# Kernel optimization log

Hardware: AMD Instinct MI355X
Metric: run time of the kernel (lower is better)

The kernel has to match this reference:

```python
import jax, jax.numpy as jnp
import numpy as np

N = 262144   # total nodes
E = 1048576  # total edges
B = 512      # graphs per batch
IN, H, EDIM, AH, CH, NB = 8, 128, 4, 128, 128, 4

def _lin(key, fi, fo):
    # kaiming_normal fan_out/relu approximated with fan_in scaling (only affects init stats)
    return jax.random.normal(key, (fi, fo), jnp.float32) * np.sqrt(2.0 / fi)

def setup_inputs() -> dict:
    key = jax.random.key(0)
    ks = jax.random.split(key, 24)
    inp = {}
    inp['x'] = jax.random.normal(ks[0], (N, IN), jnp.float32)
    inp['edge_index'] = jax.random.randint(ks[1], (2, E), 0, N)
    inp['edge_attr'] = jax.random.normal(ks[2], (E, EDIM), jnp.float32)
    seg = N // B
    inp['batch'] = (jnp.arange(N) // seg).astype(jnp.int32)
    inp['ptr'] = (jnp.arange(B + 1) * seg).astype(jnp.int32)
    dims = [(IN, H), (H, H), (H, H)]  # final layer outputs embed_dim == H
    for l, (di, do) in enumerate(dims):
        inp[f'We{l}'] = _lin(ks[3 + 2 * l], EDIM, di)
        inp[f'be{l}'] = jnp.zeros((di,), jnp.float32)
        inp[f'W{l}'] = _lin(ks[4 + 2 * l], di, do)
        inp[f'b{l}'] = jnp.zeros((do,), jnp.float32)
    inp['laW1'] = _lin(ks[10], H, AH); inp['lab1'] = jnp.zeros((AH,), jnp.float32)
    inp['laW2'] = _lin(ks[11], AH, 1); inp['lab2'] = jnp.zeros((1,), jnp.float32)
    inp['maW1'] = _lin(ks[12], H, AH); inp['mab1'] = jnp.zeros((AH,), jnp.float32)
    inp['maW2'] = _lin(ks[13], AH, NB); inp['mab2'] = jnp.zeros((NB,), jnp.float32)
    inp['lcW1'] = _lin(ks[14], H, CH); inp['lcb1'] = jnp.zeros((CH,), jnp.float32)
    inp['lcW2'] = _lin(ks[15], CH, 1); inp['lcb2'] = jnp.zeros((1,), jnp.float32)
    inp['mcW1'] = _lin(ks[16], H, CH); inp['mcb1'] = jnp.zeros((CH,), jnp.float32)
    inp['mcW2'] = _lin(ks[17], CH, 1); inp['mcb2'] = jnp.zeros((1,), jnp.float32)
    return inp

def _gnn(x, edge_index, edge_attr, Wes, bes, Ws, bs):
    # GINE-style edge-conditioned message passing (dropout off / eval mode)
    src, dst = edge_index[0], edge_index[1]
    h = x
    for We, be, W, b in zip(Wes, bes, Ws, bs):
        msg = jax.nn.relu(h[src] + edge_attr @ We + be)            # [E, d]
        agg = jax.ops.segment_sum(msg, dst, num_segments=N)        # [N, d]
        h = jax.nn.relu((h + agg) @ W + b)
    return h

def reference(x, edge_index, edge_attr, batch, ptr,
              We0, be0, W0, b0, We1, be1, W1, b1, We2, be2, W2, b2,
              laW1, lab1, laW2, lab2, maW1, mab1, maW2, mab2,
              lcW1, lcb1, lcW2, lcb2, mcW1, mcb1, mcW2, mcb2):
    emb = _gnn(x, edge_index, edge_attr, [We0, We1, We2], [be0, be1, be2], [W0, W1, W2], [b0, b1, b2])  # [N, H]

    # per-node location logit, then fused segmented softmax over each graph's nodes
    loc_logits = (jax.nn.relu(emb @ laW1 + lab1) @ laW2 + lab2)[:, 0]  # [N]
    seg_max = jax.ops.segment_max(loc_logits, batch, num_segments=B)
    shifted = loc_logits - seg_max[batch]
    denom = jax.ops.segment_sum(jnp.exp(shifted), batch, num_segments=B)
    logp = shifted - jnp.log(denom)[batch]                              # per-node log-prob within its graph
    loc_entropy = -jax.ops.segment_sum(jnp.exp(logp) * logp, batch, num_segments=B)  # [B]

    # segmented categorical sampling via Gumbel-max (global node index, matching start+local_idx)
    key = jax.random.key(42)
    u = jax.random.uniform(key, (N,), minval=1e-6, maxval=1.0 - 1e-6)
    pert = loc_logits - jnp.log(-jnp.log(u))
    pmax = jax.ops.segment_max(pert, batch, num_segments=B)
    cand = jnp.where(pert >= pmax[batch], jnp.arange(N), N)
    locations = jax.ops.segment_min(cand, batch, num_segments=B)        # [B] global indices
    loc_log_probs = logp[locations]                                     # [B]

    sel = emb[locations]                                                # [B, H]
    mut_logits = jax.nn.relu(sel @ maW1 + mab1) @ maW2 + mab2           # [B, NB]
    mut_logp = jax.nn.log_softmax(mut_logits, axis=-1)
    mutations = jax.random.categorical(jax.random.fold_in(key, 1), mut_logits, axis=-1)  # [B]
    mut_log_probs = jnp.take_along_axis(mut_logp, mutations[:, None], axis=-1)[:, 0]
    mut_entropy = -jnp.sum(jnp.exp(mut_logp) * mut_logp, axis=-1)

    # critics: global_add_pool + MLP -> scalar per graph; mutation critic on selected node
    pooled = jax.ops.segment_sum(emb, batch, num_segments=B)            # [B, H]
    loc_values = (jax.nn.relu(pooled @ lcW1 + lcb1) @ lcW2 + lcb2)[:, 0]
    mut_values = (jax.nn.relu(sel @ mcW1 + mcb1) @ mcW2 + mcb2)[:, 0]

    return (locations, mutations, loc_log_probs, mut_log_probs,
            loc_entropy, mut_entropy, loc_values, mut_values, emb)
```

## Files before the change

kernel.cpp:

```cpp
#include <hip/hip_runtime.h>
#include <cstdint>
#include <cstddef>

#define NN 262144
#define EE 1048576
#define BB 512
#define SEG 512

__device__ __forceinline__ unsigned rotl32(unsigned x, int r) {
    return (x << r) | (x >> (32 - r));
}

__device__ __forceinline__ void tf2x32(unsigned k0, unsigned k1, unsigned x0, unsigned x1,
                                       unsigned& o0, unsigned& o1) {
    unsigned ks[3] = {k0, k1, k0 ^ k1 ^ 0x1BD11BDAu};
    x0 += ks[0]; x1 += ks[1];
    const int R0[4] = {13, 15, 26, 6};
    const int R1[4] = {17, 29, 16, 24};
#pragma unroll
    for (int i = 0; i < 5; ++i) {
        const int* R = (i & 1) ? R1 : R0;
#pragma unroll
        for (int j = 0; j < 4; ++j) {
            x0 += x1;
            x1 = rotl32(x1, R[j]);
            x1 ^= x0;
        }
        x0 += ks[(i + 1) % 3];
        x1 += ks[(i + 2) % 3] + (unsigned)(i + 1);
    }
    o0 = x0; o1 = x1;
}

__device__ __forceinline__ float unif_loc(unsigned idx) {
    unsigned j = idx & (NN / 2 - 1);
    unsigned half = idx >> 17;
    unsigned o0, o1;
    tf2x32(0u, 42u, j, j + (unsigned)(NN / 2), o0, o1);
    unsigned bits = half ? o1 : o0;
    float f = __uint_as_float((bits >> 9) | 0x3F800000u) - 1.0f;
    const float minv = 1e-6f;
    const float maxv = 1.0f - 1e-6f;
    const float span = maxv - minv;
    return fmaxf(minv, __fadd_rn(__fmul_rn(f, span), minv));
}

__global__ void csr_count(const int* __restrict__ dst, int* __restrict__ counts, int E) {
    int i = blockIdx.x * 256 + threadIdx.x;
    if (i < E) atomicAdd(&counts[dst[i]], 1);
}

__global__ void scan512(const int* __restrict__ in, int* __restrict__ outExcl, int* __restrict__ bsum) {
    __shared__ int s[512];
    int b = blockIdx.x, tid = threadIdx.x;
    int v = in[(size_t)b * 512 + tid];
    s[tid] = v;
    __syncthreads();
    for (int d = 1; d < 512; d <<= 1) {
        int add = (tid >= d) ? s[tid - d] : 0;
        __syncthreads();
        s[tid] += add;
        __syncthreads();
    }
    outExcl[(size_t)b * 512 + tid] = s[tid] - v;
    if (tid == 511) bsum[b] = s[511];
}

__global__ void scan_fix(int* __restrict__ offs, const int* __restrict__ bbase,
                         int* __restrict__ cursor, int N, int E) {
    int gid = blockIdx.x * 512 + threadIdx.x;
    int v = offs[gid] + bbase[blockIdx.x];
    offs[gid] = v;
    cursor[gid] = v;
    if (gid == 0) offs[N] = E;
}

__global__ void csr_fill(const int* __restrict__ dst, const int* __restrict__ src,
                         const float4* __restrict__ ea, int* __restrict__ cursor,
                         int* __restrict__ ssrc, float4* __restrict__ sea, int E) {
    int i = blockIdx.x * 256 + threadIdx.x;
    if (i < E) {
        int p = atomicAdd(&cursor[dst[i]], 1);
        ssrc[p] = src[i];
        sea[p] = ea[i];
    }
}

__global__ void agg_l0(const float* __restrict__ x, const int* __restrict__ ssrc,
                       const float4* __restrict__ sea, const int* __restrict__ offs,
                       const float* __restrict__ We0, const float* __restrict__ be0,
                       float* __restrict__ out) {
    __shared__ float Ws[32];
    __shared__ float bs[8];
    int tid = threadIdx.x;
    if (tid < 32) Ws[tid] = We0[tid];
    if (tid < 8) bs[tid] = be0[tid];
    __syncthreads();
    int n = blockIdx.x * 256 + tid;
    float a[8] = {0.f, 0.f, 0.f, 0.f, 0.f, 0.f, 0.f, 0.f};
    int pb = offs[n], pe = offs[n + 1];
    for (int p = pb; p < pe; ++p) {
        int s = ssrc[p];
        float4 ev = sea[p];
        float4 xa = *(const float4*)(x + (size_t)s * 8);
        float4 xb = *(const float4*)(x + (size_t)s * 8 + 4);
        float xs[8] = {xa.x, xa.y, xa.z, xa.w, xb.x, xb.y, xb.z, xb.w};
#pragma unroll
        for (int j2 = 0; j2 < 8; ++j2) {
            float m = xs[j2] + bs[j2] + ev.x * Ws[j2] + ev.y * Ws[8 + j2] +
                      ev.z * Ws[16 + j2] + ev.w * Ws[24 + j2];
            a[j2] += fmaxf(m, 0.f);
        }
    }
    float4 o0 = {a[0], a[1], a[2], a[3]};
    float4 o1 = {a[4], a[5], a[6], a[7]};
    *(float4*)(out + (size_t)n * 8) = o0;
    *(float4*)(out + (size_t)n * 8 + 4) = o1;
}

__global__ __launch_bounds__(256) void update_l0(const float* __restrict__ x,
                                                 const float* __restrict__ agg0,
                                                 const float* __restrict__ W0,
                                                 const float* __restrict__ b0,
                                                 float* __restrict__ h1) {
    __shared__ float Ws[8 * 128];
    __shared__ float bs[128];
    int tid = threadIdx.x;
#pragma unroll
    for (int i = tid; i < 1024; i += 256) Ws[i] = W0[i];
    if (tid < 128) bs[tid] = b0[tid];
    __syncthreads();
    int sub = tid >> 7;
    int c = tid & 127;
    float bias = bs[c];
    float wcol[8];
#pragma unroll
    for (int k = 0; k < 8; ++k) wcol[k] = Ws[k * 128 + c];
    int base = blockIdx.x * 128;
    for (int it = 0; it < 64; ++it) {
        int node = base + it * 2 + sub;
        const float* xp = x + (size_t)node * 8;
        const float* ap = agg0 + (size_t)node * 8;
        float4 xa = *(const float4*)xp;
        float4 xb = *(const float4*)(xp + 4);
        float4 aa = *(const float4*)ap;
        float4 ab = *(const float4*)(ap + 4);
        float t[8] = {xa.x + aa.x, xa.y + aa.y, xa.z + aa.z, xa.w + aa.w,
                      xb.x + ab.x, xb.y + ab.y, xb.z + ab.z, xb.w + ab.w};
        float acc = bias;
#pragma unroll
        for (int k = 0; k < 8; ++k) acc = fmaf(t[k], wcol[k], acc);
        h1[(size_t)node * 128 + c] = fmaxf(acc, 0.f);
    }
}

__global__ __launch_bounds__(256) void agg_l(const float2* __restrict__ h2,
                                             const int* __restrict__ ssrc,
                                             const float4* __restrict__ sea,
                                             const int* __restrict__ offs,
                                             const float* __restrict__ We,
                                             const float* __restrict__ be,
                                             float2* __restrict__ out) {
    int tid = threadIdx.x;
    int lane = tid & 63;
    int n0 = blockIdx.x * 32 + (tid >> 6) * 8;
    n0 = __builtin_amdgcn_readfirstlane(n0);
    const float2* We2 = (const float2*)We;
    float2 w0 = We2[lane], w1 = We2[64 + lane], w2 = We2[128 + lane], w3 = We2[192 + lane];
    float2 bv = ((const float2*)be)[lane];

    int b0  = __builtin_amdgcn_readfirstlane(offs[n0 + 0]);
    int nb0 = __builtin_amdgcn_readfirstlane(offs[n0 + 1]);
    int nb1 = __builtin_amdgcn_readfirstlane(offs[n0 + 2]);
    int nb2 = __builtin_amdgcn_readfirstlane(offs[n0 + 3]);
    int nb3 = __builtin_amdgcn_readfirstlane(offs[n0 + 4]);
    int nb4 = __builtin_amdgcn_readfirstlane(offs[n0 + 5]);
    int nb5 = __builtin_amdgcn_readfirstlane(offs[n0 + 6]);
    int nb6 = __builtin_amdgcn_readfirstlane(offs[n0 + 7]);
    int nb7 = __builtin_amdgcn_readfirstlane(offs[n0 + 8]);
    int pend = nb7;

    float2 acc = {0.f, 0.f};
    float2* optr = out + (size_t)n0 * 64 + lane;

#define FLUSH(pp)                                        \
    while ((pp) == nb0) {                                \
        *optr = acc;                                     \
        acc.x = 0.f; acc.y = 0.f;                        \
        optr += 64;                                      \
        nb0 = nb1; nb1 = nb2; nb2 = nb3; nb3 = nb4;      \
        nb4 = nb5; nb5 = nb6; nb6 = nb7; nb7 = 0x7FFFFFFF; \
    }

#define ACC(hv, ev)                                                                     \
    {                                                                                   \
        float mx = hv.x + bv.x + ev.x * w0.x + ev.y * w1.x + ev.z * w2.x + ev.w * w3.x; \
        float my = hv.y + bv.y + ev.x * w0.y + ev.y * w1.y + ev.z * w2.y + ev.w * w3.y; \
        acc.x += fmaxf(mx, 0.f);                                                        \
        acc.y += fmaxf(my, 0.f);                                                        \
    }

    int p = b0;
    for (; p + 8 <= pend; p += 8) {
        int s_[8];
#pragma unroll
        for (int j = 0; j < 8; ++j) s_[j] = ssrc[p + j];
        float4 e_[8];
#pragma unroll
        for (int j = 0; j < 8; ++j) e_[j] = sea[p + j];
        float2 h_[8];
#pragma unroll
        for (int j = 0; j < 8; ++j) h_[j] = h2[(size_t)s_[j] * 64 + lane];
#pragma unroll
        for (int j = 0; j < 8; ++j) {
            FLUSH(p + j)
            ACC(h_[j], e_[j])
        }
    }
    for (; p < pend; ++p) {
        FLUSH(p)
        int s0 = ssrc[p];
        float4 e0 = sea[p];
        float2 ha = h2[(size_t)s0 * 64 + lane];
        ACC(ha, e0)
    }
    FLUSH(pend)
#undef ACC
#undef FLUSH
}


typedef __attribute__((ext_vector_type(8))) short bf16x8;
typedef __attribute__((ext_vector_type(4))) float f32x4;

__device__ __forceinline__ ushort bf16r(float x) {
    unsigned u = __float_as_uint(x);
    return (ushort)((u + 0x7FFFu + ((u >> 16) & 1u)) >> 16);
}
__device__ __forceinline__ float bf2f(ushort h) {
    return __uint_as_float(((unsigned)h) << 16);
}

__global__ void pack3(const float* __restrict__ W1, const float* __restrict__ W2,
                      const float* __restrict__ LA, uint4* __restrict__ dst) {
    const float* W = (blockIdx.x == 0) ? W1 : (blockIdx.x == 1) ? W2 : LA;
    uint4* ph = dst + (size_t)blockIdx.x * 4096;
    uint4* pl = ph + 2048;
    int t = threadIdx.x;
    int l = t & 63, q = t >> 6;
    int lo = l & 15, kg = l >> 4;
    for (int i = 0; i < 8; ++i) {
        int combo = q * 8 + i;
        int kc = combo >> 3, n = combo & 7;
        ushort h8[8], l8[8];
#pragma unroll
        for (int j = 0; j < 8; ++j) {
            float wv = W[(size_t)(kc * 32 + kg * 8 + j) * 128 + n * 16 + lo];
            ushort hh = bf16r(wv);
            h8[j] = hh;
            l8[j] = bf16r(wv - bf2f(hh));
        }
        int idx = (kc * 8 + n) * 64 + l;
        ph[idx] = *(const uint4*)h8;
        pl[idx] = *(const uint4*)l8;
    }
}

__device__ __forceinline__ void load_a_frags(const float* P, const float* Q, int r0,
                                             int lo, int kg, int kc,
                                             bf16x8& ah0, bf16x8& al0,
                                             bf16x8& ah1, bf16x8& al1) {
#pragma unroll
    for (int m = 0; m < 2; ++m) {
        const float* ap = P + (size_t)(r0 + m * 16 + lo) * 128 + kc * 32 + kg * 8;
        float4 p0 = *(const float4*)ap;
        float4 p1 = *(const float4*)(ap + 4);
        if (Q) {
            const float* qp = Q + (size_t)(r0 + m * 16 + lo) * 128 + kc * 32 + kg * 8;
            float4 q0 = *(const float4*)qp;
            float4 q1 = *(const float4*)(qp + 4);
            p0.x += q0.x; p0.y += q0.y; p0.z += q0.z; p0.w += q0.w;
            p1.x += q1.x; p1.y += q1.y; p1.z += q1.z; p1.w += q1.w;
        }
        float av[8] = {p0.x, p0.y, p0.z, p0.w, p1.x, p1.y, p1.z, p1.w};
        bf16x8 ah, al;
#pragma unroll
        for (int j = 0; j < 8; ++j) {
            ushort hh = bf16r(av[j]);
            ah[j] = (short)hh;
            al[j] = (short)bf16r(av[j] - bf2f(hh));
        }
        if (m == 0) { ah0 = ah; al0 = al; } else { ah1 = ah; al1 = al; }
    }
}

__global__ __launch_bounds__(256) void gemm_mfma(const float* __restrict__ P, const float* Q,
                                                 const uint4* __restrict__ Wh,
                                                 const uint4* __restrict__ Wl,
                                                 const float* __restrict__ bias,
                                                 float* out) {
    int tid = threadIdx.x;
    int w = tid >> 6, l = tid & 63;
    int r0 = blockIdx.x * 128 + w * 32;
    int lo = l & 15, kg = l >> 4;
    const bf16x8* Bh = (const bf16x8*)Wh;
    const bf16x8* Bl = (const bf16x8*)Wl;
    f32x4 acc[2][8];
#pragma unroll
    for (int m = 0; m < 2; ++m)
#pragma unroll
        for (int n = 0; n < 8; ++n) acc[m][n] = (f32x4){0.f, 0.f, 0.f, 0.f};

    for (int kc = 0; kc < 4; ++kc) {
        bf16x8 ah0, al0, ah1, al1;
        load_a_frags(P, Q, r0, lo, kg, kc, ah0, al0, ah1, al1);
#pragma unroll
        for (int h2i = 0; h2i < 2; ++h2i) {
            bf16x8 bh[4], bl[4];
#pragma unroll
            for (int nn = 0; nn < 4; ++nn) {
                int idx = (kc * 8 + h2i * 4 + nn) * 64 + l;
                bh[nn] = Bh[idx];
                bl[nn] = Bl[idx];
            }
#pragma unroll
            for (int nn = 0; nn < 4; ++nn) {
                int n = h2i * 4 + nn;
                acc[0][n] = __builtin_amdgcn_mfma_f32_16x16x32_bf16(ah0, bh[nn], acc[0][n], 0, 0, 0);
                acc[0][n] = __builtin_amdgcn_mfma_f32_16x16x32_bf16(al0, bh[nn], acc[0][n], 0, 0, 0);
                acc[0][n] = __builtin_amdgcn_mfma_f32_16x16x32_bf16(ah0, bl[nn], acc[0][n], 0, 0, 0);
                acc[1][n] = __builtin_amdgcn_mfma_f32_16x16x32_bf16(ah1, bh[nn], acc[1][n], 0, 0, 0);
                acc[1][n] = __builtin_amdgcn_mfma_f32_16x16x32_bf16(al1, bh[nn], acc[1][n], 0, 0, 0);
                acc[1][n] = __builtin_amdgcn_mfma_f32_16x16x32_bf16(ah1, bl[nn], acc[1][n], 0, 0, 0);
            }
        }
    }
    float bv[8];
#pragma unroll
    for (int n = 0; n < 8; ++n) bv[n] = bias[n * 16 + lo];
#pragma unroll
    for (int m = 0; m < 2; ++m)
#pragma unroll
        for (int n = 0; n < 8; ++n)
#pragma unroll
            for (int v = 0; v < 4; ++v) {
                size_t g = (size_t)(r0 + m * 16 + kg * 4 + v) * 128 + n * 16 + lo;
                out[g] = fmaxf(acc[m][n][v] + bv[n], 0.f);
            }
}

__global__ __launch_bounds__(256) void gemm_logit_mfma(const float* __restrict__ P,
                                                       const uint4* __restrict__ Wh,
                                                       const uint4* __restrict__ Wl,
                                                       const float* __restrict__ bias,
                                                       const float* __restrict__ w2,
                                                       const float* __restrict__ b2,
                                                       float* __restrict__ L) {
    int tid = threadIdx.x;
    int w = tid >> 6, l = tid & 63;
    int r0 = blockIdx.x * 128 + w * 32;
    int lo = l & 15, kg = l >> 4;
    const bf16x8* Bh = (const bf16x8*)Wh;
    const bf16x8* Bl = (const bf16x8*)Wl;
    f32x4 acc[2][8];
#pragma unroll
    for (int m = 0; m < 2; ++m)
#pragma unroll
        for (int n = 0; n < 8; ++n) acc[m][n] = (f32x4){0.f, 0.f, 0.f, 0.f};

    for (int kc = 0; kc < 4; ++kc) {
        bf16x8 ah0, al0, ah1, al1;
        load_a_frags(P, (const float*)0, r0, lo, kg, kc, ah0, al0, ah1, al1);
#pragma unroll
        for (int h2i = 0; h2i < 2; ++h2i) {
            bf16x8 bh[4], bl[4];
#pragma unroll
            for (int nn = 0; nn < 4; ++nn) {
                int idx = (kc * 8 + h2i * 4 + nn) * 64 + l;
                bh[nn] = Bh[idx];
                bl[nn] = Bl[idx];
            }
#pragma unroll
            for (int nn = 0; nn < 4; ++nn) {
                int n = h2i * 4 + nn;
                acc[0][n] = __builtin_amdgcn_mfma_f32_16x16x32_bf16(ah0, bh[nn], acc[0][n], 0, 0, 0);
                acc[0][n] = __builtin_amdgcn_mfma_f32_16x16x32_bf16(al0, bh[nn], acc[0][n], 0, 0, 0);
                acc[0][n] = __builtin_amdgcn_mfma_f32_16x16x32_bf16(ah0, bl[nn], acc[0][n], 0, 0, 0);
                acc[1][n] = __builtin_amdgcn_mfma_f32_16x16x32_bf16(ah1, bh[nn], acc[1][n], 0, 0, 0);
                acc[1][n] = __builtin_amdgcn_mfma_f32_16x16x32_bf16(al1, bh[nn], acc[1][n], 0, 0, 0);
                acc[1][n] = __builtin_amdgcn_mfma_f32_16x16x32_bf16(ah1, bl[nn], acc[1][n], 0, 0, 0);
            }
        }
    }
    float bv[8], w2v[8];
#pragma unroll
    for (int n = 0; n < 8; ++n) {
        bv[n] = bias[n * 16 + lo];
        w2v[n] = w2[n * 16 + lo];
    }
    float b2v = b2[0];
#pragma unroll
    for (int m = 0; m < 2; ++m)
#pragma unroll
        for (int v = 0; v < 4; ++v) {
            float s = 0.f;
#pragma unroll
            for (int n = 0; n < 8; ++n)
                s += fmaxf(acc[m][n][v] + bv[n], 0.f) * w2v[n];
            s += __shfl_xor(s, 8);
            s += __shfl_xor(s, 4);
            s += __shfl_xor(s, 2);
            s += __shfl_xor(s, 1);
            if (lo == 0) L[r0 + m * 16 + kg * 4 + v] = s + b2v;
        }
}

__global__ void sample_k(const float* __restrict__ L, float* __restrict__ ob,
                         int* __restrict__ locInt) {
    int g = blockIdx.x, tid = threadIdx.x;
    __shared__ float sh[512];
    __shared__ float rb[256];
    __shared__ int ib[256];
    float l0 = L[g * 512 + tid];
    float l1 = L[g * 512 + 256 + tid];
    rb[tid] = fmaxf(l0, l1);
    __syncthreads();
    for (int s2 = 128; s2 > 0; s2 >>= 1) {
        if (tid < s2) rb[tid] = fmaxf(rb[tid], rb[tid + s2]);
        __syncthreads();
    }
    float mx = rb[0];
    __syncthreads();
    float s0 = l0 - mx, s1 = l1 - mx;
    sh[tid] = s0; sh[256 + tid] = s1;
    float e0 = expf(s0), e1 = expf(s1);
    rb[tid] = e0 + e1;
    __syncthreads();
    for (int s2 = 128; s2 > 0; s2 >>= 1) {
        if (tid < s2) rb[tid] += rb[tid + s2];
        __syncthreads();
    }
    float denom = rb[0];
    __syncthreads();
    rb[tid] = e0 * s0 + e1 * s1;
    __syncthreads();
    for (int s2 = 128; s2 > 0; s2 >>= 1) {
        if (tid < s2) rb[tid] += rb[tid + s2];
        __syncthreads();
    }
    float sum2 = rb[0];
    __syncthreads();
    unsigned i0 = (unsigned)(g * 512 + tid);
    unsigned i1 = i0 + 256u;
    float p0 = l0 - logf(-logf(unif_loc(i0)));
    float p1 = l1 - logf(-logf(unif_loc(i1)));
    rb[tid] = fmaxf(p0, p1);
    __syncthreads();
    for (int s2 = 128; s2 > 0; s2 >>= 1) {
        if (tid < s2) rb[tid] = fmaxf(rb[tid], rb[tid + s2]);
        __syncthreads();
    }
    float pmax = rb[0];
    __syncthreads();
    int c0 = (p0 >= pmax) ? tid : 0x7FFFFFFF;
    int c1 = (p1 >= pmax) ? (tid + 256) : 0x7FFFFFFF;
    ib[tid] = min(c0, c1);
    __syncthreads();
    for (int s2 = 128; s2 > 0; s2 >>= 1) {
        if (tid < s2) ib[tid] = min(ib[tid], ib[tid + s2]);
        __syncthreads();
    }
    if (tid == 0) {
        int li = ib[0];
        float logD = logf(denom);
        ob[g] = (float)(g * 512 + li);
        ob[1024 + g] = sh[li] - logD;
        ob[2048 + g] = logD - sum2 / denom;
        locInt[g] = g * 512 + li;
    }
}

__global__ void pool_k(const float* __restrict__ emb, float* __restrict__ pooled) {
    int g = blockIdx.x, tid = threadIdx.x;
    int c = tid & 127, rg = tid >> 7;
    __shared__ float sh[512];
    float s0 = 0.f, s1 = 0.f, s2 = 0.f, s3 = 0.f;
    const float* base = emb + ((size_t)g * 512 + (size_t)rg * 128) * 128 + c;
    for (int n = 0; n < 128; n += 4) {
        s0 += base[(size_t)(n + 0) * 128];
        s1 += base[(size_t)(n + 1) * 128];
        s2 += base[(size_t)(n + 2) * 128];
        s3 += base[(size_t)(n + 3) * 128];
    }
    sh[tid] = (s0 + s1) + (s2 + s3);
    __syncthreads();
    if (rg == 0) pooled[g * 128 + c] = sh[c] + sh[128 + c] + sh[256 + c] + sh[384 + c];
}

__global__ void heads_k(const float* __restrict__ emb, const float* __restrict__ pooled,
                        const int* __restrict__ locInt,
                        const float* __restrict__ maW1, const float* __restrict__ mab1,
                        const float* __restrict__ maW2, const float* __restrict__ mab2,
                        const float* __restrict__ lcW1, const float* __restrict__ lcb1,
                        const float* __restrict__ lcW2, const float* __restrict__ lcb2,
                        const float* __restrict__ mcW1, const float* __restrict__ mcb1,
                        const float* __restrict__ mcW2, const float* __restrict__ mcb2,
                        float* __restrict__ ob) {
    int g = blockIdx.x, tid = threadIdx.x;
    __shared__ float sel[128], pl[128];
    __shared__ float red[4][128];
    __shared__ float red1[128];
    __shared__ float mcv_sh;
    sel[tid] = emb[(size_t)locInt[g] * 128 + tid];
    pl[tid] = pooled[g * 128 + tid];
    __syncthreads();
    float h = mab1[tid];
    for (int k = 0; k < 128; ++k) h = fmaf(sel[k], maW1[k * 128 + tid], h);
    h = fmaxf(h, 0.f);
    red[0][tid] = h * maW2[tid * 4 + 0];
    red[1][tid] = h * maW2[tid * 4 + 1];
    red[2][tid] = h * maW2[tid * 4 + 2];
    red[3][tid] = h * maW2[tid * 4 + 3];
    __syncthreads();
    for (int s2 = 64; s2 > 0; s2 >>= 1) {
        if (tid < s2) {
            red[0][tid] += red[0][tid + s2];
            red[1][tid] += red[1][tid + s2];
            red[2][tid] += red[2][tid + s2];
            red[3][tid] += red[3][tid + s2];
        }
        __syncthreads();
    }
    float h2 = mcb1[tid];
    for (int k = 0; k < 128; ++k) h2 = fmaf(sel[k], mcW1[k * 128 + tid], h2);
    h2 = fmaxf(h2, 0.f);
    red1[tid] = h2 * mcW2[tid];
    __syncthreads();
    for (int s2 = 64; s2 > 0; s2 >>= 1) {
        if (tid < s2) red1[tid] += red1[tid + s2];
        __syncthreads();
    }
    if (tid == 0) mcv_sh = red1[0] + mcb2[0];
    __syncthreads();
    float h3 = lcb1[tid];
    for (int k = 0; k < 128; ++k) h3 = fmaf(pl[k], lcW1[k * 128 + tid], h3);
    h3 = fmaxf(h3, 0.f);
    red1[tid] = h3 * lcW2[tid];
    __syncthreads();
    for (int s2 = 64; s2 > 0; s2 >>= 1) {
        if (tid < s2) red1[tid] += red1[tid + s2];
        __syncthreads();
    }
    if (tid == 0) {
        float lcv = red1[0] + lcb2[0];
        float lg[4];
#pragma unroll
        for (int c = 0; c < 4; ++c) lg[c] = red[c][0] + mab2[c];
        unsigned fk0, fk1;
        tf2x32(0u, 42u, 0u, 1u, fk0, fk1);
        float gmb[4];
#pragma unroll
        for (int c = 0; c < 4; ++c) {
            unsigned m = (unsigned)(g * 4 + c);
            unsigned j = m & 1023u;
            unsigned halfb = m >> 10;
            unsigned o0, o1;
            tf2x32(fk0, fk1, j, j + 1024u, o0, o1);
            unsigned bits = halfb ? o1 : o0;
            float f = __uint_as_float((bits >> 9) | 0x3F800000u) - 1.0f;
            const float tiny = 1.17549435e-38f;
            float u = fmaxf(tiny, __fadd_rn(__fmul_rn(f, 1.0f), tiny));
            gmb[c] = -logf(-logf(u));
        }
        int best = 0;
        float bz = gmb[0] + lg[0];
#pragma unroll
        for (int c = 1; c < 4; ++c) {
            float z = gmb[c] + lg[c];
            if (z > bz) { bz = z; best = c; }
        }
        float M = fmaxf(fmaxf(lg[0], lg[1]), fmaxf(lg[2], lg[3]));
        float se = 0.f;
#pragma unroll
        for (int c = 0; c < 4; ++c) se += expf(lg[c] - M);
        float lse = M + logf(se);
        float ent = 0.f;
#pragma unroll
        for (int c = 0; c < 4; ++c) {
            float lp = lg[c] - lse;
            ent -= expf(lp) * lp;
        }
        ob[512 + g] = (float)best;
        ob[1536 + g] = lg[best] - lse;
        ob[2560 + g] = ent;
        ob[3072 + g] = lcv;
        ob[3584 + g] = mcv_sh;
    }
}

extern "C" void kernel_launch(void* const* d_in, const int* in_sizes, int n_in,
                              void* d_out, int out_size, void* d_ws, size_t ws_size,
                              hipStream_t stream) {
    const float* x   = (const float*)d_in[0];
    const int* ei    = (const int*)d_in[1];
    const float* ea  = (const float*)d_in[2];
    const float* We0 = (const float*)d_in[5];
    const float* be0 = (const float*)d_in[6];
    const float* W0  = (const float*)d_in[7];
    const float* b0  = (const float*)d_in[8];
    const float* We1 = (const float*)d_in[9];
    const float* be1 = (const float*)d_in[10];
    const float* W1  = (const float*)d_in[11];
    const float* b1  = (const float*)d_in[12];
    const float* We2 = (const float*)d_in[13];
    const float* be2 = (const float*)d_in[14];
    const float* W2  = (const float*)d_in[15];
    const float* b2  = (const float*)d_in[16];
    const float* laW1 = (const float*)d_in[17];
    const float* lab1 = (const float*)d_in[18];
    const float* laW2 = (const float*)d_in[19];
    const float* lab2 = (const float*)d_in[20];
    const float* maW1 = (const float*)d_in[21];
    const float* mab1 = (const float*)d_in[22];
    const float* maW2 = (const float*)d_in[23];
    const float* mab2 = (const float*)d_in[24];
    const float* lcW1 = (const float*)d_in[25];
    const float* lcb1 = (const float*)d_in[26];
    const float* lcW2 = (const float*)d_in[27];
    const float* lcb2 = (const float*)d_in[28];
    const float* mcW1 = (const float*)d_in[29];
    const float* mcb1 = (const float*)d_in[30];
    const float* mcW2 = (const float*)d_in[31];
    const float* mcb2 = (const float*)d_in[32];

    float* out = (float*)d_out;
    char* ws = (char*)d_ws;
    size_t off = 0;
    auto alloc = [&](size_t bytes) -> void* {
        void* p = ws + off;
        off += (bytes + 255) & ~(size_t)255;
        return p;
    };
    float* U    = (float*)alloc((size_t)NN * 128 * 4);
    int* counts = (int*)alloc((size_t)NN * 4);
    int* offs   = (int*)alloc((size_t)(NN + 1) * 4);
    int* cursor = (int*)alloc((size_t)NN * 4);
    int* ssrc   = (int*)alloc((size_t)EE * 4);
    float4* sea = (float4*)alloc((size_t)EE * 16);
    int* bsum   = (int*)alloc(512 * 4);
    int* bbase  = (int*)alloc(512 * 4);
    int* bscr   = (int*)alloc(512 * 4);
    float* Lg   = (float*)alloc((size_t)NN * 4);
    float* pooled = (float*)alloc((size_t)BB * 128 * 4);
    int* locInt = (int*)alloc((size_t)BB * 4);

    const int* src = ei;
    const int* dstA = ei + EE;
    float* V = out + 4096;
    float* agg0 = U;

    uint4* wpack = (uint4*)cursor;

    hipMemsetAsync(counts, 0, (size_t)NN * 4, stream);
    csr_count<<<EE / 256, 256, 0, stream>>>(dstA, counts, EE);
    scan512<<<NN / 512, 512, 0, stream>>>(counts, offs, bsum);
    scan512<<<1, 512, 0, stream>>>(bsum, bbase, bscr);
    scan_fix<<<NN / 512, 512, 0, stream>>>(offs, bbase, cursor, NN, EE);
    csr_fill<<<EE / 256, 256, 0, stream>>>(dstA, src, (const float4*)ea, cursor, ssrc, sea, EE);
    pack3<<<3, 256, 0, stream>>>(W1, W2, laW1, wpack);

    agg_l0<<<NN / 256, 256, 0, stream>>>(x, ssrc, sea, offs, We0, be0, agg0);
    update_l0<<<NN / 128, 256, 0, stream>>>(x, agg0, W0, b0, V);
    agg_l<<<NN / 32, 256, 0, stream>>>((const float2*)V, ssrc, sea, offs, We1, be1, (float2*)U);
    gemm_mfma<<<NN / 128, 256, 0, stream>>>(V, U, wpack, wpack + 2048, b1, U);
    agg_l<<<NN / 32, 256, 0, stream>>>((const float2*)U, ssrc, sea, offs, We2, be2, (float2*)V);
    gemm_mfma<<<NN / 128, 256, 0, stream>>>(U, V, wpack + 4096, wpack + 6144, b2, V);

    gemm_logit_mfma<<<NN / 128, 256, 0, stream>>>(V, wpack + 8192, wpack + 10240, lab1, laW2, lab2, Lg);
    sample_k<<<BB, 256, 0, stream>>>(Lg, out, locInt);

    pool_k<<<BB, 512, 0, stream>>>(V, pooled);
    heads_k<<<BB, 128, 0, stream>>>(V, pooled, locInt, maW1, mab1, maW2, mab2,
                                    lcW1, lcb1, lcW2, lcb2, mcW1, mcb1, mcW2, mcb2, out);
}
```

Baseline: 888.1 us.

## Fold self term into aggregation and enlarge MFMA GEMM row tiles

The aggregation kernel now starts each node's accumulator from its own feature row h, so it writes h+agg directly. The GEMM kernels then read a single input instead of loading and adding two matrices. Each wave of the GEMM and logit kernels now covers 64 rows instead of 32, halving the grid and reusing the loaded weight fragments across four M tiles. The larger accumulator array (128 floats) raises register pressure, and launch_bounds(256,2) constrains occupancy.

```diff
diff --git a/kernel.cpp b/kernel.cpp
--- a/kernel.cpp
+++ b/kernel.cpp
@@ -180,16 +180,26 @@
     int nb7 = __builtin_amdgcn_readfirstlane(offs[n0 + 8]);
     int pend = nb7;
 
-    float2 acc = {0.f, 0.f};
+    float2 sf1 = h2[(size_t)(n0 + 1) * 64 + lane];
+    float2 sf2 = h2[(size_t)(n0 + 2) * 64 + lane];
+    float2 sf3 = h2[(size_t)(n0 + 3) * 64 + lane];
+    float2 sf4 = h2[(size_t)(n0 + 4) * 64 + lane];
+    float2 sf5 = h2[(size_t)(n0 + 5) * 64 + lane];
+    float2 sf6 = h2[(size_t)(n0 + 6) * 64 + lane];
+    float2 sf7 = h2[(size_t)(n0 + 7) * 64 + lane];
+    float2 acc = h2[(size_t)(n0 + 0) * 64 + lane];
+
     float2* optr = out + (size_t)n0 * 64 + lane;
 
-#define FLUSH(pp)                                        \
-    while ((pp) == nb0) {                                \
-        *optr = acc;                                     \
-        acc.x = 0.f; acc.y = 0.f;                        \
-        optr += 64;                                      \
-        nb0 = nb1; nb1 = nb2; nb2 = nb3; nb3 = nb4;      \
+#define FLUSH(pp)                                          \
+    while ((pp) == nb0) {                                  \
+        *optr = acc;                                       \
+        optr += 64;                                        \
+        nb0 = nb1; nb1 = nb2; nb2 = nb3; nb3 = nb4;        \
         nb4 = nb5; nb5 = nb6; nb6 = nb7; nb7 = 0x7FFFFFFF; \
+        acc = sf1;                                         \
+        sf1 = sf2; sf2 = sf3; sf3 = sf4; sf4 = sf5;        \
+        sf5 = sf6; sf6 = sf7;                              \
     }
 
 #define ACC(hv, ev)                                                                     \
@@ -266,54 +276,46 @@
     }
 }
 
-__device__ __forceinline__ void load_a_frags(const float* P, const float* Q, int r0,
-                                             int lo, int kg, int kc,
-                                             bf16x8& ah0, bf16x8& al0,
-                                             bf16x8& ah1, bf16x8& al1) {
-#pragma unroll
-    for (int m = 0; m < 2; ++m) {
-        const float* ap = P + (size_t)(r0 + m * 16 + lo) * 128 + kc * 32 + kg * 8;
-        float4 p0 = *(const float4*)ap;
-        float4 p1 = *(const float4*)(ap + 4);
-        if (Q) {
-            const float* qp = Q + (size_t)(r0 + m * 16 + lo) * 128 + kc * 32 + kg * 8;
-            float4 q0 = *(const float4*)qp;
-            float4 q1 = *(const float4*)(qp + 4);
-            p0.x += q0.x; p0.y += q0.y; p0.z += q0.z; p0.w += q0.w;
-            p1.x += q1.x; p1.y += q1.y; p1.z += q1.z; p1.w += q1.w;
-        }
-        float av[8] = {p0.x, p0.y, p0.z, p0.w, p1.x, p1.y, p1.z, p1.w};
-        bf16x8 ah, al;
-#pragma unroll
-        for (int j = 0; j < 8; ++j) {
-            ushort hh = bf16r(av[j]);
-            ah[j] = (short)hh;
-            al[j] = (short)bf16r(av[j] - bf2f(hh));
-        }
-        if (m == 0) { ah0 = ah; al0 = al; } else { ah1 = ah; al1 = al; }
-    }
-}
-
-__global__ __launch_bounds__(256) void gemm_mfma(const float* __restrict__ P, const float* Q,
-                                                 const uint4* __restrict__ Wh,
-                                                 const uint4* __restrict__ Wl,
-                                                 const float* __restrict__ bias,
-                                                 float* out) {
+__device__ __forceinline__ void conv_frag(const float4& r0, const float4& r1,
+                                          bf16x8& ah, bf16x8& al) {
+    float av[8] = {r0.x, r0.y, r0.z, r0.w, r1.x, r1.y, r1.z, r1.w};
+#pragma unroll
+    for (int j = 0; j < 8; ++j) {
+        ushort hh = bf16r(av[j]);
+        ah[j] = (short)hh;
+        al[j] = (short)bf16r(av[j] - bf2f(hh));
+    }
+}
+
+__global__ __launch_bounds__(256, 2) void gemm_mfma(const float* P,
+                                                    const uint4* __restrict__ Wh,
+                                                    const uint4* __restrict__ Wl,
+                                                    const float* __restrict__ bias,
+                                                    float* out) {
     int tid = threadIdx.x;
     int w = tid >> 6, l = tid & 63;
-    int r0 = blockIdx.x * 128 + w * 32;
+    int r0 = blockIdx.x * 256 + w * 64;
     int lo = l & 15, kg = l >> 4;
     const bf16x8* Bh = (const bf16x8*)Wh;
     const bf16x8* Bl = (const bf16x8*)Wl;
-    f32x4 acc[2][8];
-#pragma unroll
-    for (int m = 0; m < 2; ++m)
+    f32x4 acc[4][8];
+#pragma unroll
+    for (int m = 0; m < 4; ++m)
 #pragma unroll
         for (int n = 0; n < 8; ++n) acc[m][n] = (f32x4){0.f, 0.f, 0.f, 0.f};
 
     for (int kc = 0; kc < 4; ++kc) {
-        bf16x8 ah0, al0, ah1, al1;
-        load_a_frags(P, Q, r0, lo, kg, kc, ah0, al0, ah1, al1);
+        float4 pa[8];
+#pragma unroll
+        for (int m = 0; m < 4; ++m) {
+            const float* ap = P + (size_t)(r0 + m * 16 + lo) * 128 + kc * 32 + kg * 8;
+            pa[2 * m]     = *(const float4*)ap;
+            pa[2 * m + 1] = *(const float4*)(ap + 4);
+        }
+        bf16x8 ah[4], al[4];
+#pragma unroll
+        for (int m = 0; m < 4; ++m)
+            conv_frag(pa[2 * m], pa[2 * m + 1], ah[m], al[m]);
 #pragma unroll
         for (int h2i = 0; h2i < 2; ++h2i) {
             bf16x8 bh[4], bl[4];
@@ -326,12 +328,12 @@
 #pragma unroll
             for (int nn = 0; nn < 4; ++nn) {
                 int n = h2i * 4 + nn;
-                acc[0][n] = __builtin_amdgcn_mfma_f32_16x16x32_bf16(ah0, bh[nn], acc[0][n], 0, 0, 0);
-                acc[0][n] = __builtin_amdgcn_mfma_f32_16x16x32_bf16(al0, bh[nn], acc[0][n], 0, 0, 0);
-                acc[0][n] = __builtin_amdgcn_mfma_f32_16x16x32_bf16(ah0, bl[nn], acc[0][n], 0, 0, 0);
-                acc[1][n] = __builtin_amdgcn_mfma_f32_16x16x32_bf16(ah1, bh[nn], acc[1][n], 0, 0, 0);
-                acc[1][n] = __builtin_amdgcn_mfma_f32_16x16x32_bf16(al1, bh[nn], acc[1][n], 0, 0, 0);
-                acc[1][n] = __builtin_amdgcn_mfma_f32_16x16x32_bf16(ah1, bl[nn], acc[1][n], 0, 0, 0);
+#pragma unroll
+                for (int m = 0; m < 4; ++m) {
+                    acc[m][n] = __builtin_amdgcn_mfma_f32_16x16x32_bf16(ah[m], bh[nn], acc[m][n], 0, 0, 0);
+                    acc[m][n] = __builtin_amdgcn_mfma_f32_16x16x32_bf16(al[m], bh[nn], acc[m][n], 0, 0, 0);
+                    acc[m][n] = __builtin_amdgcn_mfma_f32_16x16x32_bf16(ah[m], bl[nn], acc[m][n], 0, 0, 0);
+                }
             }
         }
     }
@@ -339,7 +341,7 @@
 #pragma unroll
     for (int n = 0; n < 8; ++n) bv[n] = bias[n * 16 + lo];
 #pragma unroll
-    for (int m = 0; m < 2; ++m)
+    for (int m = 0; m < 4; ++m)
 #pragma unroll
         for (int n = 0; n < 8; ++n)
 #pragma unroll
@@ -349,28 +351,37 @@
             }
 }
 
-__global__ __launch_bounds__(256) void gemm_logit_mfma(const float* __restrict__ P,
-                                                       const uint4* __restrict__ Wh,
-                                                       const uint4* __restrict__ Wl,
-                                                       const float* __restrict__ bias,
-                                                       const float* __restrict__ w2,
-                                                       const float* __restrict__ b2,
-                                                       float* __restrict__ L) {
+__global__ __launch_bounds__(256, 2) void gemm_logit_mfma(const float* __restrict__ P,
+                                                          const uint4* __restrict__ Wh,
+                                                          const uint4* __restrict__ Wl,
+                                                          const float* __restrict__ bias,
+                                                          const float* __restrict__ w2,
+                                                          const float* __restrict__ b2,
+                                                          float* __restrict__ L) {
     int tid = threadIdx.x;
     int w = tid >> 6, l = tid & 63;
-    int r0 = blockIdx.x * 128 + w * 32;
+    int r0 = blockIdx.x * 256 + w * 64;
     int lo = l & 15, kg = l >> 4;
     const bf16x8* Bh = (const bf16x8*)Wh;
     const bf16x8* Bl = (const bf16x8*)Wl;
-    f32x4 acc[2][8];
-#pragma unroll
-    for (int m = 0; m < 2; ++m)
+    f32x4 acc[4][8];
+#pragma unroll
+    for (int m = 0; m < 4; ++m)
 #pragma unroll
         for (int n = 0; n < 8; ++n) acc[m][n] = (f32x4){0.f, 0.f, 0.f, 0.f};
 
     for (int kc = 0; kc < 4; ++kc) {
-        bf16x8 ah0, al0, ah1, al1;
-        load_a_frags(P, (const float*)0, r0, lo, kg, kc, ah0, al0, ah1, al1);
+        float4 pa[8];
+#pragma unroll
+        for (int m = 0; m < 4; ++m) {
+            const float* ap = P + (size_t)(r0 + m * 16 + lo) * 128 + kc * 32 + kg * 8;
+            pa[2 * m]     = *(const float4*)ap;
+            pa[2 * m + 1] = *(const float4*)(ap + 4);
+        }
+        bf16x8 ah[4], al[4];
+#pragma unroll
+        for (int m = 0; m < 4; ++m)
+            conv_frag(pa[2 * m], pa[2 * m + 1], ah[m], al[m]);
 #pragma unroll
         for (int h2i = 0; h2i < 2; ++h2i) {
             bf16x8 bh[4], bl[4];
@@ -383,12 +394,12 @@
 #pragma unroll
             for (int nn = 0; nn < 4; ++nn) {
                 int n = h2i * 4 + nn;
-                acc[0][n] = __builtin_amdgcn_mfma_f32_16x16x32_bf16(ah0, bh[nn], acc[0][n], 0, 0, 0);
-                acc[0][n] = __builtin_amdgcn_mfma_f32_16x16x32_bf16(al0, bh[nn], acc[0][n], 0, 0, 0);
-                acc[0][n] = __builtin_amdgcn_mfma_f32_16x16x32_bf16(ah0, bl[nn], acc[0][n], 0, 0, 0);
-                acc[1][n] = __builtin_amdgcn_mfma_f32_16x16x32_bf16(ah1, bh[nn], acc[1][n], 0, 0, 0);
-                acc[1][n] = __builtin_amdgcn_mfma_f32_16x16x32_bf16(al1, bh[nn], acc[1][n], 0, 0, 0);
-                acc[1][n] = __builtin_amdgcn_mfma_f32_16x16x32_bf16(ah1, bl[nn], acc[1][n], 0, 0, 0);
+#pragma unroll
+                for (int m = 0; m < 4; ++m) {
+                    acc[m][n] = __builtin_amdgcn_mfma_f32_16x16x32_bf16(ah[m], bh[nn], acc[m][n], 0, 0, 0);
+                    acc[m][n] = __builtin_amdgcn_mfma_f32_16x16x32_bf16(al[m], bh[nn], acc[m][n], 0, 0, 0);
+                    acc[m][n] = __builtin_amdgcn_mfma_f32_16x16x32_bf16(ah[m], bl[nn], acc[m][n], 0, 0, 0);
+                }
             }
         }
     }
@@ -400,7 +411,7 @@
     }
     float b2v = b2[0];
 #pragma unroll
-    for (int m = 0; m < 2; ++m)
+    for (int m = 0; m < 4; ++m)
 #pragma unroll
         for (int v = 0; v < 4; ++v) {
             float s = 0.f;
@@ -672,11 +683,11 @@
     agg_l0<<<NN / 256, 256, 0, stream>>>(x, ssrc, sea, offs, We0, be0, agg0);
     update_l0<<<NN / 128, 256, 0, stream>>>(x, agg0, W0, b0, V);
     agg_l<<<NN / 32, 256, 0, stream>>>((const float2*)V, ssrc, sea, offs, We1, be1, (float2*)U);
-    gemm_mfma<<<NN / 128, 256, 0, stream>>>(V, U, wpack, wpack + 2048, b1, U);
+    gemm_mfma<<<NN / 256, 256, 0, stream>>>(U, wpack, wpack + 2048, b1, U);
     agg_l<<<NN / 32, 256, 0, stream>>>((const float2*)U, ssrc, sea, offs, We2, be2, (float2*)V);
-    gemm_mfma<<<NN / 128, 256, 0, stream>>>(U, V, wpack + 4096, wpack + 6144, b2, V);
-
-    gemm_logit_mfma<<<NN / 128, 256, 0, stream>>>(V, wpack + 8192, wpack + 10240, lab1, laW2, lab2, Lg);
+    gemm_mfma<<<NN / 256, 256, 0, stream>>>(V, wpack + 4096, wpack + 6144, b2, V);
+
+    gemm_logit_mfma<<<NN / 256, 256, 0, stream>>>(V, wpack + 8192, wpack + 10240, lab1, laW2, lab2, Lg);
     sample_k<<<BB, 256, 0, stream>>>(Lg, out, locInt);
 
     pool_k<<<BB, 512, 0, stream>>>(V, pooled);
```

After: 942.8 us. 6.2% more time.

## Fuse final GNN layer GEMM with location logit head and graph pooling

Applied to the files above, without the earlier changes.

Merges the last-layer update GEMM, the location-actor logit MLP and global add pooling into one kernel. The embedding tile is staged in shared memory and fed to the second MFMA GEMM, and per-block column sums go to pooled through atomics, which needs a memset up front. This removes the separate logit GEMM and pooling kernels and two full re-reads of the embedding matrix. In exchange it adds about 68KB of shared memory per block, which may lower occupancy, and atomic accumulation makes pooled sums order-nondeterministic.

```diff
diff --git a/kernel.cpp b/kernel.cpp
--- a/kernel.cpp
+++ b/kernel.cpp
@@ -229,7 +229,6 @@
 #undef FLUSH
 }
 
-
 typedef __attribute__((ext_vector_type(8))) short bf16x8;
 typedef __attribute__((ext_vector_type(4))) float f32x4;
 
@@ -266,6 +265,17 @@
     }
 }
 
+__device__ __forceinline__ void conv_frag(const float4& r0, const float4& r1,
+                                          bf16x8& ah, bf16x8& al) {
+    float av[8] = {r0.x, r0.y, r0.z, r0.w, r1.x, r1.y, r1.z, r1.w};
+#pragma unroll
+    for (int j = 0; j < 8; ++j) {
+        ushort hh = bf16r(av[j]);
+        ah[j] = (short)hh;
+        al[j] = (short)bf16r(av[j] - bf2f(hh));
+    }
+}
+
 __device__ __forceinline__ void load_a_frags(const float* P, const float* Q, int r0,
                                              int lo, int kg, int kc,
                                              bf16x8& ah0, bf16x8& al0,
@@ -282,14 +292,8 @@
             p0.x += q0.x; p0.y += q0.y; p0.z += q0.z; p0.w += q0.w;
             p1.x += q1.x; p1.y += q1.y; p1.z += q1.z; p1.w += q1.w;
         }
-        float av[8] = {p0.x, p0.y, p0.z, p0.w, p1.x, p1.y, p1.z, p1.w};
         bf16x8 ah, al;
-#pragma unroll
-        for (int j = 0; j < 8; ++j) {
-            ushort hh = bf16r(av[j]);
-            ah[j] = (short)hh;
-            al[j] = (short)bf16r(av[j] - bf2f(hh));
-        }
+        conv_frag(p0, p1, ah, al);
         if (m == 0) { ah0 = ah; al0 = al; } else { ah1 = ah; al1 = al; }
     }
 }
@@ -349,13 +353,20 @@
             }
 }
 
-__global__ __launch_bounds__(256) void gemm_logit_mfma(const float* __restrict__ P,
-                                                       const uint4* __restrict__ Wh,
-                                                       const uint4* __restrict__ Wl,
-                                                       const float* __restrict__ bias,
-                                                       const float* __restrict__ w2,
-                                                       const float* __restrict__ b2,
-                                                       float* __restrict__ L) {
+__global__ __launch_bounds__(256) void gemm_emb_fused(const float* __restrict__ P, const float* Q,
+                                                      const uint4* __restrict__ Wh,
+                                                      const uint4* __restrict__ Wl,
+                                                      const float* __restrict__ bias,
+                                                      const uint4* __restrict__ LWh,
+                                                      const uint4* __restrict__ LWl,
+                                                      const float* __restrict__ lb1,
+                                                      const float* __restrict__ lw2,
+                                                      const float* __restrict__ lb2,
+                                                      float* out,
+                                                      float* __restrict__ pooled,
+                                                      float* __restrict__ Lg) {
+    __shared__ float eL[4][32][132];
+    __shared__ float poolL[4][128];
     int tid = threadIdx.x;
     int w = tid >> 6, l = tid & 63;
     int r0 = blockIdx.x * 128 + w * 32;
@@ -370,7 +381,7 @@
 
     for (int kc = 0; kc < 4; ++kc) {
         bf16x8 ah0, al0, ah1, al1;
-        load_a_frags(P, (const float*)0, r0, lo, kg, kc, ah0, al0, ah1, al1);
+        load_a_frags(P, Q, r0, lo, kg, kc, ah0, al0, ah1, al1);
 #pragma unroll
         for (int h2i = 0; h2i < 2; ++h2i) {
             bf16x8 bh[4], bl[4];
@@ -392,13 +403,82 @@
             }
         }
     }
-    float bv[8], w2v[8];
+    float bv[8];
+#pragma unroll
+    for (int n = 0; n < 8; ++n) bv[n] = bias[n * 16 + lo];
+    float psum[8];
+#pragma unroll
+    for (int n = 0; n < 8; ++n) psum[n] = 0.f;
+#pragma unroll
+    for (int m = 0; m < 2; ++m)
+#pragma unroll
+        for (int n = 0; n < 8; ++n)
+#pragma unroll
+            for (int v = 0; v < 4; ++v) {
+                float e = fmaxf(acc[m][n][v] + bv[n], 0.f);
+                size_t g = (size_t)(r0 + m * 16 + kg * 4 + v) * 128 + n * 16 + lo;
+                out[g] = e;
+                eL[w][m * 16 + kg * 4 + v][n * 16 + lo] = e;
+                psum[n] += e;
+            }
 #pragma unroll
     for (int n = 0; n < 8; ++n) {
-        bv[n] = bias[n * 16 + lo];
-        w2v[n] = w2[n * 16 + lo];
-    }
-    float b2v = b2[0];
+        psum[n] += __shfl_xor(psum[n], 16);
+        psum[n] += __shfl_xor(psum[n], 32);
+    }
+    if (l < 16) {
+#pragma unroll
+        for (int n = 0; n < 8; ++n) poolL[w][n * 16 + l] = psum[n];
+    }
+    __syncthreads();
+    if (tid < 128) {
+        float s = poolL[0][tid] + poolL[1][tid] + poolL[2][tid] + poolL[3][tid];
+        atomicAdd(&pooled[(blockIdx.x >> 2) * 128 + tid], s);
+    }
+    const bf16x8* LBh = (const bf16x8*)LWh;
+    const bf16x8* LBl = (const bf16x8*)LWl;
+    f32x4 acc2[2][8];
+#pragma unroll
+    for (int m = 0; m < 2; ++m)
+#pragma unroll
+        for (int n = 0; n < 8; ++n) acc2[m][n] = (f32x4){0.f, 0.f, 0.f, 0.f};
+    for (int kc = 0; kc < 4; ++kc) {
+        bf16x8 ah[2], al[2];
+#pragma unroll
+        for (int m = 0; m < 2; ++m) {
+            const float* ep = &eL[w][m * 16 + lo][kc * 32 + kg * 8];
+            float4 a0 = *(const float4*)ep;
+            float4 a1 = *(const float4*)(ep + 4);
+            conv_frag(a0, a1, ah[m], al[m]);
+        }
+#pragma unroll
+        for (int h2i = 0; h2i < 2; ++h2i) {
+            bf16x8 bh[4], bl[4];
+#pragma unroll
+            for (int nn = 0; nn < 4; ++nn) {
+                int idx = (kc * 8 + h2i * 4 + nn) * 64 + l;
+                bh[nn] = LBh[idx];
+                bl[nn] = LBl[idx];
+            }
+#pragma unroll
+            for (int nn = 0; nn < 4; ++nn) {
+                int n = h2i * 4 + nn;
+                acc2[0][n] = __builtin_amdgcn_mfma_f32_16x16x32_bf16(ah[0], bh[nn], acc2[0][n], 0, 0, 0);
+                acc2[0][n] = __builtin_amdgcn_mfma_f32_16x16x32_bf16(al[0], bh[nn], acc2[0][n], 0, 0, 0);
+                acc2[0][n] = __builtin_amdgcn_mfma_f32_16x16x32_bf16(ah[0], bl[nn], acc2[0][n], 0, 0, 0);
+                acc2[1][n] = __builtin_amdgcn_mfma_f32_16x16x32_bf16(ah[1], bh[nn], acc2[1][n], 0, 0, 0);
+                acc2[1][n] = __builtin_amdgcn_mfma_f32_16x16x32_bf16(al[1], bh[nn], acc2[1][n], 0, 0, 0);
+                acc2[1][n] = __builtin_amdgcn_mfma_f32_16x16x32_bf16(ah[1], bl[nn], acc2[1][n], 0, 0, 0);
+            }
+        }
+    }
+    float b1v[8], w2v[8];
+#pragma unroll
+    for (int n = 0; n < 8; ++n) {
+        b1v[n] = lb1[n * 16 + lo];
+        w2v[n] = lw2[n * 16 + lo];
+    }
+    float lb2v = lb2[0];
 #pragma unroll
     for (int m = 0; m < 2; ++m)
 #pragma unroll
@@ -406,12 +486,12 @@
             float s = 0.f;
 #pragma unroll
             for (int n = 0; n < 8; ++n)
-                s += fmaxf(acc[m][n][v] + bv[n], 0.f) * w2v[n];
+                s += fmaxf(acc2[m][n][v] + b1v[n], 0.f) * w2v[n];
             s += __shfl_xor(s, 8);
             s += __shfl_xor(s, 4);
             s += __shfl_xor(s, 2);
             s += __shfl_xor(s, 1);
-            if (lo == 0) L[r0 + m * 16 + kg * 4 + v] = s + b2v;
+            if (lo == 0) Lg[r0 + m * 16 + kg * 4 + v] = s + lb2v;
         }
 }
 
@@ -478,23 +558,6 @@
         ob[2048 + g] = logD - sum2 / denom;
         locInt[g] = g * 512 + li;
     }
-}
-
-__global__ void pool_k(const float* __restrict__ emb, float* __restrict__ pooled) {
-    int g = blockIdx.x, tid = threadIdx.x;
-    int c = tid & 127, rg = tid >> 7;
-    __shared__ float sh[512];
-    float s0 = 0.f, s1 = 0.f, s2 = 0.f, s3 = 0.f;
-    const float* base = emb + ((size_t)g * 512 + (size_t)rg * 128) * 128 + c;
-    for (int n = 0; n < 128; n += 4) {
-        s0 += base[(size_t)(n + 0) * 128];
-        s1 += base[(size_t)(n + 1) * 128];
-        s2 += base[(size_t)(n + 2) * 128];
-        s3 += base[(size_t)(n + 3) * 128];
-    }
-    sh[tid] = (s0 + s1) + (s2 + s3);
-    __syncthreads();
-    if (rg == 0) pooled[g * 128 + c] = sh[c] + sh[128 + c] + sh[256 + c] + sh[384 + c];
 }
 
 __global__ void heads_k(const float* __restrict__ emb, const float* __restrict__ pooled,
@@ -662,6 +725,7 @@
     uint4* wpack = (uint4*)cursor;
 
     hipMemsetAsync(counts, 0, (size_t)NN * 4, stream);
+    hipMemsetAsync(pooled, 0, (size_t)BB * 128 * 4, stream);
     csr_count<<<EE / 256, 256, 0, stream>>>(dstA, counts, EE);
     scan512<<<NN / 512, 512, 0, stream>>>(counts, offs, bsum);
     scan512<<<1, 512, 0, stream>>>(bsum, bbase, bscr);
@@ -674,12 +738,11 @@
     agg_l<<<NN / 32, 256, 0, stream>>>((const float2*)V, ssrc, sea, offs, We1, be1, (float2*)U);
     gemm_mfma<<<NN / 128, 256, 0, stream>>>(V, U, wpack, wpack + 2048, b1, U);
     agg_l<<<NN / 32, 256, 0, stream>>>((const float2*)U, ssrc, sea, offs, We2, be2, (float2*)V);
-    gemm_mfma<<<NN / 128, 256, 0, stream>>>(U, V, wpack + 4096, wpack + 6144, b2, V);
-
-    gemm_logit_mfma<<<NN / 128, 256, 0, stream>>>(V, wpack + 8192, wpack + 10240, lab1, laW2, lab2, Lg);
+    gemm_emb_fused<<<NN / 128, 256, 0, stream>>>(U, V, wpack + 4096, wpack + 6144, b2,
+                                                 wpack + 8192, wpack + 10240, lab1, laW2, lab2,
+                                                 V, pooled, Lg);
+
     sample_k<<<BB, 256, 0, stream>>>(Lg, out, locInt);
-
-    pool_k<<<BB, 512, 0, stream>>>(V, pooled);
     heads_k<<<BB, 128, 0, stream>>>(V, pooled, locInt, maW1, mab1, maW2, mab2,
                                     lcW1, lcb1, lcW2, lcb2, mcW1, mcb1, mcW2, mcb2, out);
 }
```

Result: faster. 854.9 us (-3.7%).
